# Kernel tuning notes

Measured on AMD Instinct MI355X. Metric: run time of the kernel, lower is better.

The kernel has to match this reference:

```python
import jax, jax.numpy as jnp
import numpy as np

N = 100000      # nodes
E = 1200000     # edges
D_IN = 128      # input_dim
H = 64          # hidden_dim
OUT = 3         # output_dim
EPS = 1e-5      # BatchNorm eps


def setup_inputs() -> dict:
    key = jax.random.key(0)
    ks = jax.random.split(key, 24)
    w = lambda k, shape: jax.random.normal(k, shape, jnp.float32) * 0.05
    return {
        "x": jax.random.normal(ks[0], (N, D_IN), jnp.float32),
        "edge_index": jax.random.randint(ks[1], (2, E), 0, N, dtype=jnp.int32),
        "proj_W": w(ks[2], (H, D_IN)), "proj_b": w(ks[3], (H,)),
        "conv1_W": w(ks[4], (H, H)), "conv1_b": w(ks[5], (H,)),
        "bn1_g": jnp.ones((H,), jnp.float32), "bn1_b": w(ks[6], (H,)),
        "conv2_W": w(ks[7], (H, H)), "conv2_b": w(ks[8], (H,)),
        "bn2_g": jnp.ones((H,), jnp.float32), "bn2_b": w(ks[9], (H,)),
        "conv3_W": w(ks[10], (H, H)), "conv3_b": w(ks[11], (H,)),
        "bn3_g": jnp.ones((H,), jnp.float32), "bn3_b": w(ks[12], (H,)),
        "byp_W": w(ks[13], (OUT, D_IN)), "byp_b": w(ks[14], (OUT,)),
        "head_W": w(ks[15], (OUT, H + OUT)), "head_b": w(ks[16], (OUT,)),
    }


def reference(x, edge_index, proj_W, proj_b,
              conv1_W, conv1_b, bn1_g, bn1_b,
              conv2_W, conv2_b, bn2_g, bn2_b,
              conv3_W, conv3_b, bn3_g, bn3_b,
              byp_W, byp_b, head_W, head_b):
    n = x.shape[0]
    row, col = edge_index[0], edge_index[1]
    loop = jnp.arange(n, dtype=row.dtype)
    row_f = jnp.concatenate([row, loop])   # source (with self loops)
    col_f = jnp.concatenate([col, loop])   # target
    # symmetric GCN normalization: deg over targets of A+I, edge weight 1
    deg = jax.ops.segment_sum(jnp.ones(row_f.shape, jnp.float32), col_f, num_segments=n)
    dinv = jnp.where(deg > 0, jax.lax.rsqrt(deg), 0.0)
    norm = dinv[row_f] * dinv[col_f]       # [E+N]

    def gcn(h, W, b):
        h = h @ W.T                                    # transform then propagate
        msg = h[row_f] * norm[:, None]                 # gather + scale
        return jax.ops.segment_sum(msg, col_f, num_segments=n) + b

    def bn(h, g, b):
        # eval-mode BatchNorm1d: running_mean=0, running_var=1 buffers
        return h * (g / jnp.sqrt(1.0 + EPS)) + b

    h = x @ proj_W.T + proj_b
    idn = h
    h = jax.nn.relu(bn(gcn(h, conv1_W, conv1_b), bn1_g, bn1_b)) + idn  # dropout inactive (eval)
    idn = h
    h = jax.nn.relu(bn(gcn(h, conv2_W, conv2_b), bn2_g, bn2_b)) + idn
    h = jax.nn.relu(bn(gcn(h, conv3_W, conv3_b), bn3_g, bn3_b))

    byp = x @ byp_W.T + byp_b
    p = jnp.concatenate([h, byp], axis=1) @ head_W.T + head_b
    kappa = jnp.clip(p[:, 0] * 5.0 + 2.5, 0.2, 10.0)
    alpha = p[:, 1]
    tau = jnp.clip(p[:, 2] + 0.5, 0.05, 2.0)
    return jnp.stack([kappa, alpha, tau], axis=1)
```

## Files before the change

kernel.cpp:

```cpp
#include <hip/hip_runtime.h>
#include <hip/hip_fp16.h>

#define NN 100000
#define NE 1200000
#define NBUK ((NN + 127) / 128)
#define NCHUNK 512

typedef _Float16 h8 __attribute__((ext_vector_type(8)));
typedef float f32x4 __attribute__((ext_vector_type(4)));
typedef float f32x2 __attribute__((ext_vector_type(2)));

__global__ __launch_bounds__(256) void k_bucketA(const int* __restrict__ col,
                                                 int* __restrict__ blkcnt,
                                                 int* __restrict__ bcnt) {
    __shared__ int lh[NBUK];
    const int tid = threadIdx.x;
    const int per = (NE + NCHUNK - 1) / NCHUNK;
    const int e0 = blockIdx.x * per;
    const int e1 = (e0 + per < NE) ? (e0 + per) : NE;
    for (int i = tid; i < NBUK; i += 256) lh[i] = 0;
    __syncthreads();
    for (int e = e0 + tid; e < e1; e += 256)
        atomicAdd(&lh[col[e] >> 7], 1);
    __syncthreads();
    for (int b = tid; b < NBUK; b += 256) {
        int v = lh[b];
        blkcnt[b * NCHUNK + blockIdx.x] = v;
        if (v) atomicAdd(&bcnt[b], v);
    }
}

__global__ __launch_bounds__(1024) void k_scanAll(int* __restrict__ blkcnt,
                                                  int* __restrict__ bcnt) {
    __shared__ int s[1024];
    const int b = blockIdx.x, tid = threadIdx.x;
    if (b < NBUK) {
        int v = (tid < NCHUNK) ? blkcnt[b * NCHUNK + tid] : 0;
        s[tid] = v;
        __syncthreads();
        #pragma unroll
        for (int d = 1; d < 1024; d <<= 1) {
            int t = (tid >= d) ? s[tid - d] : 0;
            __syncthreads();
            s[tid] += t;
            __syncthreads();
        }
        if (tid < NCHUNK) blkcnt[b * NCHUNK + tid] = s[tid] - v;
    } else {
        int v = (tid < NBUK) ? bcnt[tid] : 0;
        s[tid] = v;
        __syncthreads();
        #pragma unroll
        for (int d = 1; d < 1024; d <<= 1) {
            int t = (tid >= d) ? s[tid - d] : 0;
            __syncthreads();
            s[tid] += t;
            __syncthreads();
        }
        if (tid < NBUK) bcnt[tid] = s[tid] - v;
        if (tid == 0) bcnt[NBUK] = NE;
    }
}

__global__ __launch_bounds__(256) void k_bucketB(const int* __restrict__ row,
                                                 const int* __restrict__ col,
                                                 const int* __restrict__ bbase,
                                                 const int* __restrict__ blkcnt,
                                                 unsigned* __restrict__ tmp) {
    __shared__ int lh[NBUK];
    const int tid = threadIdx.x;
    const int per = (NE + NCHUNK - 1) / NCHUNK;
    const int e0 = blockIdx.x * per;
    const int e1 = (e0 + per < NE) ? (e0 + per) : NE;
    for (int b = tid; b < NBUK; b += 256)
        lh[b] = bbase[b] + blkcnt[b * NCHUNK + blockIdx.x];
    __syncthreads();
    for (int e = e0 + tid; e < e1; e += 256) {
        int c = col[e], r = row[e];
        int pos = atomicAdd(&lh[c >> 7], 1);
        tmp[pos] = ((unsigned)r << 7) | (unsigned)(c & 127);
    }
}

__global__ __launch_bounds__(256) void k_build(const unsigned* __restrict__ tmp,
                                               const int* __restrict__ bbase,
                                               int* __restrict__ off,
                                               float* __restrict__ dinv,
                                               int* __restrict__ csr_row) {
    __shared__ int cnt[128], s[128], cur[128];
    const int b = blockIdx.x, tid = threadIdx.x;
    const int colBase = b << 7;
    const int nCols = (NN - colBase < 128) ? (NN - colBase) : 128;
    const int seg0 = bbase[b], seg1 = bbase[b + 1];
    if (tid < 128) cnt[tid] = 0;
    __syncthreads();
    for (int i = seg0 + tid; i < seg1; i += 256)
        atomicAdd(&cnt[tmp[i] & 127], 1);
    __syncthreads();
    if (tid < 128) s[tid] = cnt[tid];
    __syncthreads();
    #pragma unroll
    for (int d = 1; d < 128; d <<= 1) {
        int t = (tid < 128 && tid >= d) ? s[tid - d] : 0;
        __syncthreads();
        if (tid < 128) s[tid] += t;
        __syncthreads();
    }
    if (tid < nCols) {
        int exc = seg0 + s[tid] - cnt[tid];
        off[colBase + tid] = exc;
        cur[tid] = exc;
        dinv[colBase + tid] = rsqrtf((float)cnt[tid] + 1.0f);
    }
    if (b == 0 && tid == 0) off[NN] = NE;
    __syncthreads();
    for (int i = seg0 + tid; i < seg1; i += 256) {
        unsigned v = tmp[i];
        int pos = atomicAdd(&cur[v & 127u], 1);
        csr_row[pos] = (int)(v >> 7);
    }
}

__global__ __launch_bounds__(256) void k_gemmPC(const float* __restrict__ X,
                                                const float* __restrict__ W,
                                                const float* __restrict__ bias,
                                                _Float16* __restrict__ Yh,
                                                const float* __restrict__ bypW,
                                                const float* __restrict__ bypb,
                                                float* __restrict__ bypOut,
                                                const float* __restrict__ convW1,
                                                const float* __restrict__ dinv,
                                                unsigned char* __restrict__ Y8,
                                                int n_nodes) {
    constexpr int D = 128, RS = D + 8, KS = D / 32;
    constexpr int RS2 = 72;
    __shared__ _Float16 Xh[64 * RS];
    __shared__ _Float16 Wh[64 * RS];
    const int tid = threadIdx.x;
    const int n0 = blockIdx.x * 64;

    for (int i = tid; i < 64 * (D / 8); i += 256) {
        int j = i / (D / 8), d8 = (i % (D / 8)) * 8;
        const float4* wp = (const float4*)&W[j * D + d8];
        float4 w0 = wp[0], w1 = wp[1];
        h8 h = { (_Float16)w0.x, (_Float16)w0.y, (_Float16)w0.z, (_Float16)w0.w,
                 (_Float16)w1.x, (_Float16)w1.y, (_Float16)w1.z, (_Float16)w1.w };
        *(h8*)&Wh[j * RS + d8] = h;
    }
    for (int i = tid; i < 64 * (D / 8); i += 256) {
        int nl = i / (D / 8), d8 = (i % (D / 8)) * 8;
        int n = n0 + nl; if (n >= n_nodes) n = n_nodes - 1;
        const float4* xp = (const float4*)&X[(size_t)n * D + d8];
        float4 x0 = xp[0], x1 = xp[1];
        h8 h = { (_Float16)x0.x, (_Float16)x0.y, (_Float16)x0.z, (_Float16)x0.w,
                 (_Float16)x1.x, (_Float16)x1.y, (_Float16)x1.z, (_Float16)x1.w };
        *(h8*)&Xh[nl * RS + d8] = h;
    }
    __syncthreads();

    const int wid = tid >> 6, lane = tid & 63;
    const int lm = lane & 15, lq = lane >> 4;
    const int mBase = wid * 16;

    h8 bfrag[4][KS];
    #pragma unroll
    for (int t = 0; t < 4; ++t)
        #pragma unroll
        for (int s = 0; s < KS; ++s)
            bfrag[t][s] = *(const h8*)&Wh[(t * 16 + lm) * RS + s * 32 + lq * 8];

    h8 bfragB[KS];
    #pragma unroll
    for (int s = 0; s < KS; ++s) {
        if (lm < 3) {
            const float4* wp = (const float4*)&bypW[lm * D + s * 32 + lq * 8];
            float4 w0 = wp[0], w1 = wp[1];
            bfragB[s] = (h8){ (_Float16)w0.x, (_Float16)w0.y, (_Float16)w0.z, (_Float16)w0.w,
                              (_Float16)w1.x, (_Float16)w1.y, (_Float16)w1.z, (_Float16)w1.w };
        } else {
            bfragB[s] = (h8)(_Float16)0;
        }
    }

    f32x4 acc[5] = {};
    #pragma unroll
    for (int s = 0; s < KS; ++s) {
        h8 a = *(const h8*)&Xh[(mBase + lm) * RS + s * 32 + lq * 8];
        #pragma unroll
        for (int t = 0; t < 4; ++t)
            acc[t] = __builtin_amdgcn_mfma_f32_16x16x32_f16(a, bfrag[t][s], acc[t], 0, 0, 0);
        acc[4] = __builtin_amdgcn_mfma_f32_16x16x32_f16(a, bfragB[s], acc[4], 0, 0, 0);
    }

    float bb[4];
    #pragma unroll
    for (int t = 0; t < 4; ++t) bb[t] = bias[t * 16 + lm];
    float bypbv = (lm < 3) ? bypb[lm] : 0.f;
    const int nodeBase = n0 + mBase + lq * 4;

    __syncthreads();

    #pragma unroll
    for (int r = 0; r < 4; ++r) {
        int node = nodeBase + r;
        int nloc = mBase + lq * 4 + r;
        #pragma unroll
        for (int t = 0; t < 4; ++t) {
            _Float16 hv = (_Float16)(acc[t][r] + bb[t]);
            Xh[nloc * RS2 + t * 16 + lm] = hv;
            if (node < n_nodes)
                Yh[(size_t)node * 64 + t * 16 + lm] = hv;
        }
        if (node < n_nodes && lm < 3)
            bypOut[node * 3 + lm] = acc[4][r] + bypbv;
    }
    for (int i = tid; i < 64 * 8; i += 256) {
        int j = i >> 3, d8 = (i & 7) * 8;
        const float4* wp = (const float4*)&convW1[j * 64 + d8];
        float4 w0 = wp[0], w1 = wp[1];
        h8 h = { (_Float16)w0.x, (_Float16)w0.y, (_Float16)w0.z, (_Float16)w0.w,
                 (_Float16)w1.x, (_Float16)w1.y, (_Float16)w1.z, (_Float16)w1.w };
        *(h8*)&Wh[j * RS2 + d8] = h;
    }
    __syncthreads();

    h8 cfrag[4][2];
    #pragma unroll
    for (int t = 0; t < 4; ++t)
        #pragma unroll
        for (int s = 0; s < 2; ++s)
            cfrag[t][s] = *(const h8*)&Wh[(t * 16 + lm) * RS2 + s * 32 + lq * 8];

    f32x4 acc2[4] = {};
    #pragma unroll
    for (int s = 0; s < 2; ++s) {
        h8 a = *(const h8*)&Xh[(mBase + lm) * RS2 + s * 32 + lq * 8];
        #pragma unroll
        for (int t = 0; t < 4; ++t)
            acc2[t] = __builtin_amdgcn_mfma_f32_16x16x32_f16(a, cfrag[t][s], acc2[t], 0, 0, 0);
    }
    #pragma unroll
    for (int r = 0; r < 4; ++r) {
        int node = nodeBase + r;
        if (node < n_nodes) {
            float sdv = dinv[node];
            #pragma unroll
            for (int t = 0; t < 4; ++t) {
                float v = acc2[t][r] * sdv;
                int pk = __builtin_amdgcn_cvt_pk_fp8_f32(v, v, 0, false);
                Y8[(size_t)node * 64 + t * 16 + lm] = (unsigned char)(pk & 0xff);
            }
        }
    }
}

__device__ __forceinline__ void acc8(float* acc, uint2 w) {
    f32x2 p0 = __builtin_amdgcn_cvt_pk_f32_fp8(w.x, false);
    f32x2 p1 = __builtin_amdgcn_cvt_pk_f32_fp8(w.x, true);
    f32x2 p2 = __builtin_amdgcn_cvt_pk_f32_fp8(w.y, false);
    f32x2 p3 = __builtin_amdgcn_cvt_pk_f32_fp8(w.y, true);
    acc[0] += p0.x; acc[1] += p0.y; acc[2] += p1.x; acc[3] += p1.y;
    acc[4] += p2.x; acc[5] += p2.y; acc[6] += p3.x; acc[7] += p3.y;
}

template<bool HEAD>
__global__ __launch_bounds__(256) void k_gather(const unsigned char* __restrict__ hB8,
                                                const float* __restrict__ dinv,
                                                const int* __restrict__ off,
                                                const int* __restrict__ csr_row,
                                                const float* __restrict__ convb,
                                                const float* __restrict__ bng,
                                                const float* __restrict__ bnb,
                                                _Float16* __restrict__ hA,
                                                const float* __restrict__ nextW,
                                                unsigned char* __restrict__ Y8,
                                                const float* __restrict__ byp,
                                                const float* __restrict__ headW,
                                                const float* __restrict__ headb,
                                                float* __restrict__ out) {
    constexpr int RS2 = 72;
    __shared__ _Float16 Ws[HEAD ? 1 : 64 * RS2];
    __shared__ _Float16 Hs[HEAD ? 1 : 32 * RS2];
    __shared__ float HWs[HEAD ? 204 : 1];
    const int tid = threadIdx.x;
    if constexpr (HEAD) {
        for (int i = tid; i < 204; i += 256)
            HWs[i] = (i < 201) ? headW[i] : headb[i - 201];
        __syncthreads();
    } else {
        for (int i = tid; i < 64 * 8; i += 256) {
            int j = i >> 3, d8 = (i & 7) * 8;
            const float4* wp = (const float4*)&nextW[j * 64 + d8];
            float4 w0 = wp[0], w1 = wp[1];
            h8 h = { (_Float16)w0.x, (_Float16)w0.y, (_Float16)w0.z, (_Float16)w0.w,
                     (_Float16)w1.x, (_Float16)w1.y, (_Float16)w1.z, (_Float16)w1.w };
            *(h8*)&Ws[j * RS2 + d8] = h;
        }
    }
    const int wid = tid >> 6, lane = tid & 63;
    const int nloc = wid * 8 + (lane >> 3);
    const int n = blockIdx.x * 32 + nloc;
    const int oct = lane & 7;
    const int f0 = oct * 8;
    const int ngb = lane & 56;

    const int e0 = off[n];
    const int deg = off[n + 1] - e0;

    const uint2* rows8 = (const uint2*)hB8;

    int ip0, ip1, ip2, ip3;
    {
        int a0 = e0 + oct;      ip0 = csr_row[a0 < NE ? a0 : NE - 1];
        int a1 = e0 + 8 + oct;  ip1 = csr_row[a1 < NE ? a1 : NE - 1];
        int a2 = e0 + 16 + oct; ip2 = csr_row[a2 < NE ? a2 : NE - 1];
        int a3 = e0 + 24 + oct; ip3 = csr_row[a3 < NE ? a3 : NE - 1];
    }

    float acc[8] = {0, 0, 0, 0, 0, 0, 0, 0};
    acc8(acc, rows8[(size_t)n * 8 + oct]);

    auto process16 = [&](int iA, int iB, int base) {
        uint2 w[16];
        #pragma unroll
        for (int q = 0; q < 8; ++q) {
            int rq = __shfl(iA, ngb | q, 64);
            rq = (base + q < deg) ? rq : n;
            w[q] = rows8[(size_t)rq * 8 + oct];
        }
        #pragma unroll
        for (int q = 8; q < 16; ++q) {
            int rq = __shfl(iB, ngb | (q - 8), 64);
            rq = (base + q < deg) ? rq : n;
            w[q] = rows8[(size_t)rq * 8 + oct];
        }
        #pragma unroll
        for (int q = 0; q < 16; ++q) {
            if (base + q >= deg) { w[q].x = 0; w[q].y = 0; }
            acc8(acc, w[q]);
        }
    };
    if (deg > 0)  process16(ip0, ip1, 0);
    if (deg > 16) process16(ip2, ip3, 16);
    for (int it = 32; it < deg; it += 8) {
        uint2 w[8];
        #pragma unroll
        for (int q = 0; q < 8; ++q) {
            int rq = csr_row[(it + q < deg) ? e0 + it + q : e0];
            w[q] = rows8[(size_t)rq * 8 + oct];
            if (it + q >= deg) { w[q].x = 0; w[q].y = 0; }
        }
        #pragma unroll
        for (int q = 0; q < 8; ++q) acc8(acc, w[q]);
    }

    const float dv = dinv[n];
    const float bnscale = rsqrtf(1.0f + 1e-5f);
    const float4 cb0 = *(const float4*)&convb[f0], cb1 = *(const float4*)&convb[f0 + 4];
    const float4 g0  = *(const float4*)&bng[f0],  g1  = *(const float4*)&bng[f0 + 4];
    const float4 b0_ = *(const float4*)&bnb[f0],  b1_ = *(const float4*)&bnb[f0 + 4];
    const float cb[8] = { cb0.x, cb0.y, cb0.z, cb0.w, cb1.x, cb1.y, cb1.z, cb1.w };
    const float gg[8] = { g0.x, g0.y, g0.z, g0.w, g1.x, g1.y, g1.z, g1.w };
    const float bb[8] = { b0_.x, b0_.y, b0_.z, b0_.w, b1_.x, b1_.y, b1_.z, b1_.w };
    float v[8];
    #pragma unroll
    for (int j = 0; j < 8; ++j)
        v[j] = fmaxf((acc[j] * dv + cb[j]) * (gg[j] * bnscale) + bb[j], 0.0f);

    if constexpr (!HEAD) {
        size_t o = ((size_t)n << 6) + f0;
        h8 old = *(const h8*)&hA[o];
        #pragma unroll
        for (int j = 0; j < 8; ++j) v[j] += (float)old[j];
        h8 res = { (_Float16)v[0], (_Float16)v[1], (_Float16)v[2], (_Float16)v[3],
                   (_Float16)v[4], (_Float16)v[5], (_Float16)v[6], (_Float16)v[7] };
        *(h8*)&hA[o] = res;
        *(h8*)&Hs[nloc * RS2 + f0] = res;
        __syncthreads();

        const int lm = lane & 15, lq = lane >> 4;
        const int mt = (wid & 1) * 16;
        const int nt = (wid >> 1) * 32;
        h8 afrag[2], bfrag[2][2];
        #pragma unroll
        for (int s = 0; s < 2; ++s)
            afrag[s] = *(const h8*)&Hs[(mt + lm) * RS2 + s * 32 + lq * 8];
        #pragma unroll
        for (int t = 0; t < 2; ++t)
            #pragma unroll
            for (int s = 0; s < 2; ++s)
                bfrag[t][s] = *(const h8*)&Ws[(nt + t * 16 + lm) * RS2 + s * 32 + lq * 8];
        f32x4 acc2[2] = {};
        #pragma unroll
        for (int s = 0; s < 2; ++s)
            #pragma unroll
            for (int t = 0; t < 2; ++t)
                acc2[t] = __builtin_amdgcn_mfma_f32_16x16x32_f16(afrag[s], bfrag[t][s], acc2[t], 0, 0, 0);
        const int nodeBase = blockIdx.x * 32 + mt + lq * 4;
        #pragma unroll
        for (int r = 0; r < 4; ++r) {
            int node = nodeBase + r;
            float sdv = dinv[node];
            #pragma unroll
            for (int t = 0; t < 2; ++t) {
                float vv = acc2[t][r] * sdv;
                int pk = __builtin_amdgcn_cvt_pk_fp8_f32(vv, vv, 0, false);
                Y8[(size_t)node * 64 + nt + t * 16 + lm] = (unsigned char)(pk & 0xff);
            }
        }
    } else {
        float p[3];
        #pragma unroll
        for (int o = 0; o < 3; ++o) {
            float t = 0.f;
            #pragma unroll
            for (int j = 0; j < 8; ++j) t += v[j] * HWs[o * 67 + f0 + j];
            p[o] = t;
        }
        #pragma unroll
        for (int mask = 1; mask < 8; mask <<= 1) {
            #pragma unroll
            for (int o = 0; o < 3; ++o) p[o] += __shfl_xor(p[o], mask, 64);
        }
        if (oct == 0) {
            float by0 = byp[n * 3], by1 = byp[n * 3 + 1], by2 = byp[n * 3 + 2];
            #pragma unroll
            for (int o = 0; o < 3; ++o)
                p[o] += by0 * HWs[o * 67 + 64] + by1 * HWs[o * 67 + 65] + by2 * HWs[o * 67 + 66]
                      + HWs[201 + o];
            float kappa = fminf(fmaxf(p[0] * 5.0f + 2.5f, 0.2f), 10.0f);
            float tau   = fminf(fmaxf(p[2] + 0.5f, 0.05f), 2.0f);
            out[(size_t)n * 3]     = kappa;
            out[(size_t)n * 3 + 1] = p[1];
            out[(size_t)n * 3 + 2] = tau;
        }
    }
}

extern "C" void kernel_launch(void* const* d_in, const int* in_sizes, int n_in,
                              void* d_out, int out_size, void* d_ws, size_t ws_size,
                              hipStream_t stream) {
    const float* x     = (const float*)d_in[0];
    const int*   ei    = (const int*)d_in[1];
    const int*   row   = ei;
    const int*   col   = ei + NE;
    const float* projW = (const float*)d_in[2];
    const float* projb = (const float*)d_in[3];
    const float* convW[3] = { (const float*)d_in[4], (const float*)d_in[8],  (const float*)d_in[12] };
    const float* convb[3] = { (const float*)d_in[5], (const float*)d_in[9],  (const float*)d_in[13] };
    const float* bng[3]   = { (const float*)d_in[6], (const float*)d_in[10], (const float*)d_in[14] };
    const float* bnb[3]   = { (const float*)d_in[7], (const float*)d_in[11], (const float*)d_in[15] };
    const float* bypW  = (const float*)d_in[16];
    const float* bypb  = (const float*)d_in[17];
    const float* headW = (const float*)d_in[18];
    const float* headb = (const float*)d_in[19];
    float* out = (float*)d_out;

    float*    ws   = (float*)d_ws;
    float*    dinv = ws;
    _Float16* hAh  = (_Float16*)(ws + 102400);
    unsigned char* hB8a = (unsigned char*)(hAh + (size_t)NN * 64);
    float*    byp  = (float*)(hB8a + (size_t)NN * 64);
    int*      off     = (int*)(byp + 300032);
    int*      csr_row = off + 100096;
    int*      bcnt    = csr_row + NE;
    int*      blkcnt  = bcnt + 784;
    unsigned char* hB8b = (unsigned char*)(blkcnt + (size_t)NBUK * NCHUNK);
    unsigned* tmp     = (unsigned*)hAh;

    hipMemsetAsync(bcnt, 0, 784 * sizeof(int), stream);
    k_bucketA<<<NCHUNK, 256, 0, stream>>>(col, blkcnt, bcnt);
    k_scanAll<<<NBUK + 1, 1024, 0, stream>>>(blkcnt, bcnt);
    k_bucketB<<<NCHUNK, 256, 0, stream>>>(row, col, bcnt, blkcnt, tmp);
    k_build<<<NBUK, 256, 0, stream>>>(tmp, bcnt, off, dinv, csr_row);

    k_gemmPC<<<(NN + 63) / 64, 256, 0, stream>>>(
        x, projW, projb, hAh, bypW, bypb, byp, convW[0], dinv, hB8a, NN);

    k_gather<false><<<NN / 32, 256, 0, stream>>>(
        hB8a, dinv, off, csr_row, convb[0], bng[0], bnb[0], hAh,
        convW[1], hB8b, nullptr, nullptr, nullptr, nullptr);
    k_gather<false><<<NN / 32, 256, 0, stream>>>(
        hB8b, dinv, off, csr_row, convb[1], bng[1], bnb[1], hAh,
        convW[2], hB8a, nullptr, nullptr, nullptr, nullptr);
    k_gather<true><<<NN / 32, 256, 0, stream>>>(
        hB8a, dinv, off, csr_row, convb[2], bng[2], bnb[2], nullptr,
        nullptr, nullptr, byp, headW, headb, out);
}
```

Measured before the change: 260.1 us.

## Drop memset and global bucket atomics; make gather blocks loop over node tiles

Removes the hipMemsetAsync and the global atomic accumulation of per-bucket counts. Each scan block now writes its own bucket total, and the bucket base offsets are recomputed redundantly inside k_bucketB (block-wide scan) and k_build (prefix reduction). The gather kernels now process 4 tiles of 32 nodes per block, so the shared-memory weight conversion is amortised across tiles. This costs an extra barrier per tile and fewer blocks for latency hiding. The redundant prefix computations add a little work per block in exchange for one fewer launch and no atomics.

```diff
diff --git a/kernel.cpp b/kernel.cpp
--- a/kernel.cpp
+++ b/kernel.cpp
@@ -5,14 +5,15 @@
 #define NE 1200000
 #define NBUK ((NN + 127) / 128)
 #define NCHUNK 512
+#define NTILE 3125
+#define TPB 4
 
 typedef _Float16 h8 __attribute__((ext_vector_type(8)));
 typedef float f32x4 __attribute__((ext_vector_type(4)));
 typedef float f32x2 __attribute__((ext_vector_type(2)));
 
 __global__ __launch_bounds__(256) void k_bucketA(const int* __restrict__ col,
-                                                 int* __restrict__ blkcnt,
-                                                 int* __restrict__ bcnt) {
+                                                 int* __restrict__ blkcnt) {
     __shared__ int lh[NBUK];
     const int tid = threadIdx.x;
     const int per = (NE + NCHUNK - 1) / NCHUNK;
@@ -23,58 +24,63 @@
     for (int e = e0 + tid; e < e1; e += 256)
         atomicAdd(&lh[col[e] >> 7], 1);
     __syncthreads();
-    for (int b = tid; b < NBUK; b += 256) {
-        int v = lh[b];
-        blkcnt[b * NCHUNK + blockIdx.x] = v;
-        if (v) atomicAdd(&bcnt[b], v);
-    }
+    for (int b = tid; b < NBUK; b += 256)
+        blkcnt[b * NCHUNK + blockIdx.x] = lh[b];
 }
 
 __global__ __launch_bounds__(1024) void k_scanAll(int* __restrict__ blkcnt,
                                                   int* __restrict__ bcnt) {
     __shared__ int s[1024];
     const int b = blockIdx.x, tid = threadIdx.x;
-    if (b < NBUK) {
-        int v = (tid < NCHUNK) ? blkcnt[b * NCHUNK + tid] : 0;
-        s[tid] = v;
-        __syncthreads();
-        #pragma unroll
-        for (int d = 1; d < 1024; d <<= 1) {
-            int t = (tid >= d) ? s[tid - d] : 0;
-            __syncthreads();
-            s[tid] += t;
-            __syncthreads();
-        }
-        if (tid < NCHUNK) blkcnt[b * NCHUNK + tid] = s[tid] - v;
-    } else {
-        int v = (tid < NBUK) ? bcnt[tid] : 0;
-        s[tid] = v;
-        __syncthreads();
-        #pragma unroll
-        for (int d = 1; d < 1024; d <<= 1) {
-            int t = (tid >= d) ? s[tid - d] : 0;
-            __syncthreads();
-            s[tid] += t;
-            __syncthreads();
-        }
-        if (tid < NBUK) bcnt[tid] = s[tid] - v;
-        if (tid == 0) bcnt[NBUK] = NE;
-    }
+    int v = (tid < NCHUNK) ? blkcnt[b * NCHUNK + tid] : 0;
+    s[tid] = v;
+    __syncthreads();
+    #pragma unroll
+    for (int d = 1; d < 1024; d <<= 1) {
+        int t = (tid >= d) ? s[tid - d] : 0;
+        __syncthreads();
+        s[tid] += t;
+        __syncthreads();
+    }
+    if (tid < NCHUNK) blkcnt[b * NCHUNK + tid] = s[tid] - v;
+    if (tid == 1023) bcnt[b] = s[1023];
 }
 
 __global__ __launch_bounds__(256) void k_bucketB(const int* __restrict__ row,
                                                  const int* __restrict__ col,
-                                                 const int* __restrict__ bbase,
+                                                 const int* __restrict__ bcnt,
                                                  const int* __restrict__ blkcnt,
                                                  unsigned* __restrict__ tmp) {
     __shared__ int lh[NBUK];
+    __shared__ int part[256];
     const int tid = threadIdx.x;
+    int loc[4]; int sum = 0;
+    #pragma unroll
+    for (int j = 0; j < 4; ++j) {
+        int idx = tid * 4 + j;
+        loc[j] = sum;
+        sum += (idx < NBUK) ? bcnt[idx] : 0;
+    }
+    part[tid] = sum;
+    __syncthreads();
+    #pragma unroll
+    for (int d = 1; d < 256; d <<= 1) {
+        int t = (tid >= d) ? part[tid - d] : 0;
+        __syncthreads();
+        part[tid] += t;
+        __syncthreads();
+    }
+    const int excl = part[tid] - sum;
+    #pragma unroll
+    for (int j = 0; j < 4; ++j) {
+        int idx = tid * 4 + j;
+        if (idx < NBUK)
+            lh[idx] = excl + loc[j] + blkcnt[idx * NCHUNK + blockIdx.x];
+    }
+    __syncthreads();
     const int per = (NE + NCHUNK - 1) / NCHUNK;
     const int e0 = blockIdx.x * per;
     const int e1 = (e0 + per < NE) ? (e0 + per) : NE;
-    for (int b = tid; b < NBUK; b += 256)
-        lh[b] = bbase[b] + blkcnt[b * NCHUNK + blockIdx.x];
-    __syncthreads();
     for (int e = e0 + tid; e < e1; e += 256) {
         int c = col[e], r = row[e];
         int pos = atomicAdd(&lh[c >> 7], 1);
@@ -83,15 +89,26 @@
 }
 
 __global__ __launch_bounds__(256) void k_build(const unsigned* __restrict__ tmp,
-                                               const int* __restrict__ bbase,
+                                               const int* __restrict__ bcnt,
                                                int* __restrict__ off,
                                                float* __restrict__ dinv,
                                                int* __restrict__ csr_row) {
     __shared__ int cnt[128], s[128], cur[128];
+    __shared__ int red[256];
     const int b = blockIdx.x, tid = threadIdx.x;
+    int ssum = 0;
+    for (int i = tid; i < b; i += 256) ssum += bcnt[i];
+    red[tid] = ssum;
+    __syncthreads();
+    #pragma unroll
+    for (int d = 128; d > 0; d >>= 1) {
+        if (tid < d) red[tid] += red[tid + d];
+        __syncthreads();
+    }
+    const int seg0 = red[0];
+    const int seg1 = seg0 + bcnt[b];
     const int colBase = b << 7;
     const int nCols = (NN - colBase < 128) ? (NN - colBase) : 128;
-    const int seg0 = bbase[b], seg1 = bbase[b + 1];
     if (tid < 128) cnt[tid] = 0;
     __syncthreads();
     for (int i = seg0 + tid; i < seg1; i += 256)
@@ -299,140 +316,146 @@
     }
     const int wid = tid >> 6, lane = tid & 63;
     const int nloc = wid * 8 + (lane >> 3);
-    const int n = blockIdx.x * 32 + nloc;
     const int oct = lane & 7;
     const int f0 = oct * 8;
     const int ngb = lane & 56;
-
-    const int e0 = off[n];
-    const int deg = off[n + 1] - e0;
-
+    const float bnscale = rsqrtf(1.0f + 1e-5f);
     const uint2* rows8 = (const uint2*)hB8;
 
-    int ip0, ip1, ip2, ip3;
-    {
-        int a0 = e0 + oct;      ip0 = csr_row[a0 < NE ? a0 : NE - 1];
-        int a1 = e0 + 8 + oct;  ip1 = csr_row[a1 < NE ? a1 : NE - 1];
-        int a2 = e0 + 16 + oct; ip2 = csr_row[a2 < NE ? a2 : NE - 1];
-        int a3 = e0 + 24 + oct; ip3 = csr_row[a3 < NE ? a3 : NE - 1];
-    }
-
-    float acc[8] = {0, 0, 0, 0, 0, 0, 0, 0};
-    acc8(acc, rows8[(size_t)n * 8 + oct]);
-
-    auto process16 = [&](int iA, int iB, int base) {
-        uint2 w[16];
+    #pragma unroll 1
+    for (int tt = 0; tt < TPB; ++tt) {
+        const int tile = blockIdx.x * TPB + tt;
+        if (tile >= NTILE) break;
+        const int n = tile * 32 + nloc;
+
+        const int e0 = off[n];
+        const int deg = off[n + 1] - e0;
+
+        int ip0, ip1, ip2, ip3;
+        {
+            int a0 = e0 + oct;      ip0 = csr_row[a0 < NE ? a0 : NE - 1];
+            int a1 = e0 + 8 + oct;  ip1 = csr_row[a1 < NE ? a1 : NE - 1];
+            int a2 = e0 + 16 + oct; ip2 = csr_row[a2 < NE ? a2 : NE - 1];
+            int a3 = e0 + 24 + oct; ip3 = csr_row[a3 < NE ? a3 : NE - 1];
+        }
+
+        float acc[8] = {0, 0, 0, 0, 0, 0, 0, 0};
+        acc8(acc, rows8[(size_t)n * 8 + oct]);
+
+        auto process16 = [&](int iA, int iB, int base) {
+            uint2 w[16];
+            #pragma unroll
+            for (int q = 0; q < 8; ++q) {
+                int rq = __shfl(iA, ngb | q, 64);
+                rq = (base + q < deg) ? rq : n;
+                w[q] = rows8[(size_t)rq * 8 + oct];
+            }
+            #pragma unroll
+            for (int q = 8; q < 16; ++q) {
+                int rq = __shfl(iB, ngb | (q - 8), 64);
+                rq = (base + q < deg) ? rq : n;
+                w[q] = rows8[(size_t)rq * 8 + oct];
+            }
+            #pragma unroll
+            for (int q = 0; q < 16; ++q) {
+                if (base + q >= deg) { w[q].x = 0; w[q].y = 0; }
+                acc8(acc, w[q]);
+            }
+        };
+        if (deg > 0)  process16(ip0, ip1, 0);
+        if (deg > 16) process16(ip2, ip3, 16);
+        for (int it = 32; it < deg; it += 8) {
+            uint2 w[8];
+            #pragma unroll
+            for (int q = 0; q < 8; ++q) {
+                int rq = csr_row[(it + q < deg) ? e0 + it + q : e0];
+                w[q] = rows8[(size_t)rq * 8 + oct];
+                if (it + q >= deg) { w[q].x = 0; w[q].y = 0; }
+            }
+            #pragma unroll
+            for (int q = 0; q < 8; ++q) acc8(acc, w[q]);
+        }
+
+        const float dv = dinv[n];
+        const float4 cb0 = *(const float4*)&convb[f0], cb1 = *(const float4*)&convb[f0 + 4];
+        const float4 g0  = *(const float4*)&bng[f0],  g1  = *(const float4*)&bng[f0 + 4];
+        const float4 b0_ = *(const float4*)&bnb[f0],  b1_ = *(const float4*)&bnb[f0 + 4];
+        const float cb[8] = { cb0.x, cb0.y, cb0.z, cb0.w, cb1.x, cb1.y, cb1.z, cb1.w };
+        const float gg[8] = { g0.x, g0.y, g0.z, g0.w, g1.x, g1.y, g1.z, g1.w };
+        const float bb[8] = { b0_.x, b0_.y, b0_.z, b0_.w, b1_.x, b1_.y, b1_.z, b1_.w };
+        float v[8];
         #pragma unroll
-        for (int q = 0; q < 8; ++q) {
-            int rq = __shfl(iA, ngb | q, 64);
-            rq = (base + q < deg) ? rq : n;
-            w[q] = rows8[(size_t)rq * 8 + oct];
-        }
-        #pragma unroll
-        for (int q = 8; q < 16; ++q) {
-            int rq = __shfl(iB, ngb | (q - 8), 64);
-            rq = (base + q < deg) ? rq : n;
-            w[q] = rows8[(size_t)rq * 8 + oct];
-        }
-        #pragma unroll
-        for (int q = 0; q < 16; ++q) {
-            if (base + q >= deg) { w[q].x = 0; w[q].y = 0; }
-            acc8(acc, w[q]);
-        }
-    };
-    if (deg > 0)  process16(ip0, ip1, 0);
-    if (deg > 16) process16(ip2, ip3, 16);
-    for (int it = 32; it < deg; it += 8) {
-        uint2 w[8];
-        #pragma unroll
-        for (int q = 0; q < 8; ++q) {
-            int rq = csr_row[(it + q < deg) ? e0 + it + q : e0];
-            w[q] = rows8[(size_t)rq * 8 + oct];
-            if (it + q >= deg) { w[q].x = 0; w[q].y = 0; }
-        }
-        #pragma unroll
-        for (int q = 0; q < 8; ++q) acc8(acc, w[q]);
-    }
-
-    const float dv = dinv[n];
-    const float bnscale = rsqrtf(1.0f + 1e-5f);
-    const float4 cb0 = *(const float4*)&convb[f0], cb1 = *(const float4*)&convb[f0 + 4];
-    const float4 g0  = *(const float4*)&bng[f0],  g1  = *(const float4*)&bng[f0 + 4];
-    const float4 b0_ = *(const float4*)&bnb[f0],  b1_ = *(const float4*)&bnb[f0 + 4];
-    const float cb[8] = { cb0.x, cb0.y, cb0.z, cb0.w, cb1.x, cb1.y, cb1.z, cb1.w };
-    const float gg[8] = { g0.x, g0.y, g0.z, g0.w, g1.x, g1.y, g1.z, g1.w };
-    const float bb[8] = { b0_.x, b0_.y, b0_.z, b0_.w, b1_.x, b1_.y, b1_.z, b1_.w };
-    float v[8];
-    #pragma unroll
-    for (int j = 0; j < 8; ++j)
-        v[j] = fmaxf((acc[j] * dv + cb[j]) * (gg[j] * bnscale) + bb[j], 0.0f);
-
-    if constexpr (!HEAD) {
-        size_t o = ((size_t)n << 6) + f0;
-        h8 old = *(const h8*)&hA[o];
-        #pragma unroll
-        for (int j = 0; j < 8; ++j) v[j] += (float)old[j];
-        h8 res = { (_Float16)v[0], (_Float16)v[1], (_Float16)v[2], (_Float16)v[3],
-                   (_Float16)v[4], (_Float16)v[5], (_Float16)v[6], (_Float16)v[7] };
-        *(h8*)&hA[o] = res;
-        *(h8*)&Hs[nloc * RS2 + f0] = res;
-        __syncthreads();
-
-        const int lm = lane & 15, lq = lane >> 4;
-        const int mt = (wid & 1) * 16;
-        const int nt = (wid >> 1) * 32;
-        h8 afrag[2], bfrag[2][2];
-        #pragma unroll
-        for (int s = 0; s < 2; ++s)
-            afrag[s] = *(const h8*)&Hs[(mt + lm) * RS2 + s * 32 + lq * 8];
-        #pragma unroll
-        for (int t = 0; t < 2; ++t)
+        for (int j = 0; j < 8; ++j)
+            v[j] = fmaxf((acc[j] * dv + cb[j]) * (gg[j] * bnscale) + bb[j], 0.0f);
+
+        if constexpr (!HEAD) {
+            size_t o = ((size_t)n << 6) + f0;
+            h8 old = *(const h8*)&hA[o];
+            #pragma unroll
+            for (int j = 0; j < 8; ++j) v[j] += (float)old[j];
+            h8 res = { (_Float16)v[0], (_Float16)v[1], (_Float16)v[2], (_Float16)v[3],
+                       (_Float16)v[4], (_Float16)v[5], (_Float16)v[6], (_Float16)v[7] };
+            *(h8*)&hA[o] = res;
+            *(h8*)&Hs[nloc * RS2 + f0] = res;
+            __syncthreads();
+
+            const int lm = lane & 15, lq = lane >> 4;
+            const int mt = (wid & 1) * 16;
+            const int nt = (wid >> 1) * 32;
+            h8 afrag[2], bfrag[2][2];
             #pragma unroll
             for (int s = 0; s < 2; ++s)
-                bfrag[t][s] = *(const h8*)&Ws[(nt + t * 16 + lm) * RS2 + s * 32 + lq * 8];
-        f32x4 acc2[2] = {};
-        #pragma unroll
-        for (int s = 0; s < 2; ++s)
+                afrag[s] = *(const h8*)&Hs[(mt + lm) * RS2 + s * 32 + lq * 8];
             #pragma unroll
             for (int t = 0; t < 2; ++t)
-                acc2[t] = __builtin_amdgcn_mfma_f32_16x16x32_f16(afrag[s], bfrag[t][s], acc2[t], 0, 0, 0);
-        const int nodeBase = blockIdx.x * 32 + mt + lq * 4;
-        #pragma unroll
-        for (int r = 0; r < 4; ++r) {
-            int node = nodeBase + r;
-            float sdv = dinv[node];
-            #pragma unroll
-            for (int t = 0; t < 2; ++t) {
-                float vv = acc2[t][r] * sdv;
-                int pk = __builtin_amdgcn_cvt_pk_fp8_f32(vv, vv, 0, false);
-                Y8[(size_t)node * 64 + nt + t * 16 + lm] = (unsigned char)(pk & 0xff);
-            }
-        }
-    } else {
-        float p[3];
-        #pragma unroll
-        for (int o = 0; o < 3; ++o) {
-            float t = 0.f;
-            #pragma unroll
-            for (int j = 0; j < 8; ++j) t += v[j] * HWs[o * 67 + f0 + j];
-            p[o] = t;
-        }
-        #pragma unroll
-        for (int mask = 1; mask < 8; mask <<= 1) {
-            #pragma unroll
-            for (int o = 0; o < 3; ++o) p[o] += __shfl_xor(p[o], mask, 64);
-        }
-        if (oct == 0) {
-            float by0 = byp[n * 3], by1 = byp[n * 3 + 1], by2 = byp[n * 3 + 2];
-            #pragma unroll
-            for (int o = 0; o < 3; ++o)
-                p[o] += by0 * HWs[o * 67 + 64] + by1 * HWs[o * 67 + 65] + by2 * HWs[o * 67 + 66]
-                      + HWs[201 + o];
-            float kappa = fminf(fmaxf(p[0] * 5.0f + 2.5f, 0.2f), 10.0f);
-            float tau   = fminf(fmaxf(p[2] + 0.5f, 0.05f), 2.0f);
-            out[(size_t)n * 3]     = kappa;
-            out[(size_t)n * 3 + 1] = p[1];
-            out[(size_t)n * 3 + 2] = tau;
+                #pragma unroll
+                for (int s = 0; s < 2; ++s)
+                    bfrag[t][s] = *(const h8*)&Ws[(nt + t * 16 + lm) * RS2 + s * 32 + lq * 8];
+            f32x4 acc2[2] = {};
+            #pragma unroll
+            for (int s = 0; s < 2; ++s)
+                #pragma unroll
+                for (int t = 0; t < 2; ++t)
+                    acc2[t] = __builtin_amdgcn_mfma_f32_16x16x32_f16(afrag[s], bfrag[t][s], acc2[t], 0, 0, 0);
+            const int nodeBase = tile * 32 + mt + lq * 4;
+            #pragma unroll
+            for (int r = 0; r < 4; ++r) {
+                int node = nodeBase + r;
+                float sdv = dinv[node];
+                #pragma unroll
+                for (int t = 0; t < 2; ++t) {
+                    float vv = acc2[t][r] * sdv;
+                    int pk = __builtin_amdgcn_cvt_pk_fp8_f32(vv, vv, 0, false);
+                    Y8[(size_t)node * 64 + nt + t * 16 + lm] = (unsigned char)(pk & 0xff);
+                }
+            }
+            __syncthreads();
+        } else {
+            float p[3];
+            #pragma unroll
+            for (int o2 = 0; o2 < 3; ++o2) {
+                float t = 0.f;
+                #pragma unroll
+                for (int j = 0; j < 8; ++j) t += v[j] * HWs[o2 * 67 + f0 + j];
+                p[o2] = t;
+            }
+            #pragma unroll
+            for (int mask = 1; mask < 8; mask <<= 1) {
+                #pragma unroll
+                for (int o2 = 0; o2 < 3; ++o2) p[o2] += __shfl_xor(p[o2], mask, 64);
+            }
+            if (oct == 0) {
+                float by0 = byp[n * 3], by1 = byp[n * 3 + 1], by2 = byp[n * 3 + 2];
+                #pragma unroll
+                for (int o2 = 0; o2 < 3; ++o2)
+                    p[o2] += by0 * HWs[o2 * 67 + 64] + by1 * HWs[o2 * 67 + 65]
+                           + by2 * HWs[o2 * 67 + 66] + HWs[201 + o2];
+                float kappa = fminf(fmaxf(p[0] * 5.0f + 2.5f, 0.2f), 10.0f);
+                float tau   = fminf(fmaxf(p[2] + 0.5f, 0.05f), 2.0f);
+                out[(size_t)n * 3]     = kappa;
+                out[(size_t)n * 3 + 1] = p[1];
+                out[(size_t)n * 3 + 2] = tau;
+            }
         }
     }
 }
@@ -468,22 +491,22 @@
     unsigned char* hB8b = (unsigned char*)(blkcnt + (size_t)NBUK * NCHUNK);
     unsigned* tmp     = (unsigned*)hAh;
 
-    hipMemsetAsync(bcnt, 0, 784 * sizeof(int), stream);
-    k_bucketA<<<NCHUNK, 256, 0, stream>>>(col, blkcnt, bcnt);
-    k_scanAll<<<NBUK + 1, 1024, 0, stream>>>(blkcnt, bcnt);
+    k_bucketA<<<NCHUNK, 256, 0, stream>>>(col, blkcnt);
+    k_scanAll<<<NBUK, 1024, 0, stream>>>(blkcnt, bcnt);
     k_bucketB<<<NCHUNK, 256, 0, stream>>>(row, col, bcnt, blkcnt, tmp);
     k_build<<<NBUK, 256, 0, stream>>>(tmp, bcnt, off, dinv, csr_row);
 
     k_gemmPC<<<(NN + 63) / 64, 256, 0, stream>>>(
         x, projW, projb, hAh, bypW, bypb, byp, convW[0], dinv, hB8a, NN);
 
-    k_gather<false><<<NN / 32, 256, 0, stream>>>(
+    const int GBLK = (NTILE + TPB - 1) / TPB;
+    k_gather<false><<<GBLK, 256, 0, stream>>>(
         hB8a, dinv, off, csr_row, convb[0], bng[0], bnb[0], hAh,
         convW[1], hB8b, nullptr, nullptr, nullptr, nullptr);
-    k_gather<false><<<NN / 32, 256, 0, stream>>>(
+    k_gather<false><<<GBLK, 256, 0, stream>>>(
         hB8b, dinv, off, csr_row, convb[1], bng[1], bnb[1], hAh,
         convW[2], hB8a, nullptr, nullptr, nullptr, nullptr);
-    k_gather<true><<<NN / 32, 256, 0, stream>>>(
+    k_gather<true><<<GBLK, 256, 0, stream>>>(
         hB8a, dinv, off, csr_row, convb[2], bng[2], bnb[2], nullptr,
         nullptr, nullptr, byp, headW, headb, out);
 }
```

Measured after the change: 265.8 us. +2.2%, slower.
